# Kernel optimization log

Measured on AMD Instinct MI355X. Metric: run time of the kernel, lower is better.

Reference implementation:

```python
import jax, jax.numpy as jnp
import numpy as np

DAMPENING = 50.0
THR = 1.0
TAU = 10.0
DECAY = float(np.exp(-1.0 / TAU))
V_MIN = -1.0


@jax.custom_vjp
def spike_fn(v_scaled):
    # Heaviside spike with surrogate (triangular) gradient
    return (v_scaled > 0.0).astype(v_scaled.dtype)

def _spike_fwd(v_scaled):
    return spike_fn(v_scaled), v_scaled

def _spike_bwd(v_scaled, dy):
    return (dy * DAMPENING * jnp.maximum(0.0, 1.0 - jnp.abs(v_scaled)),)

spike_fn.defvjp(_spike_fwd, _spike_bwd)


def setup_inputs() -> dict:
    key = jax.random.key(0)
    T, B, N_IN, N = 256, 32, 256, 2048
    ks = jax.random.split(key, 4)
    x = jax.random.normal(ks[0], (T, B, N_IN), jnp.float32)
    W_in = jax.random.normal(ks[1], (N_IN, N), jnp.float32) * (1.0 / np.sqrt(N_IN))
    b = jnp.zeros((N,), jnp.float32)
    # original uses stddev 1/sqrt(n_in) for Bernoulli_weights as well
    W_bern = jax.random.normal(ks[2], (N, N), jnp.float32) * (1.0 / np.sqrt(N_IN))
    random_indices = jax.random.randint(ks[3], (T, N), 0, N)
    return {"x": x, "W_in": W_in, "b": b, "W_bern": W_bern,
            "random_indices": random_indices}


def reference(x, W_in, b, W_bern, random_indices):
    # x: [T, B, n_in]; states v, z2: [B, n]
    B, N = x.shape[1], W_in.shape[1]
    v0 = jnp.zeros((B, N), x.dtype)
    z2_0 = jnp.zeros((B, N), x.dtype)  # old_spike state (unused in math, as in original)

    def step(carry, inp):
        v, _old_z2 = carry
        xt, idx = inp
        i_in = xt @ W_in + b                               # [B, n]
        new_v = jnp.clip(DECAY * v + i_in, V_MIN, THR + 0.01)
        z = spike_fn(new_v - THR)                          # spikes [B, n]
        new_v = jnp.where(z > 0.0, V_MIN, new_v)           # hard reset
        z2 = jnp.take(z @ W_bern, idx, axis=1)             # stochastic projection + column gather
        return (new_v, z2), (z, new_v, z2)

    _, (zs, vs, z2s) = jax.lax.scan(step, (v0, z2_0), (x, random_indices))
    return jnp.stack([zs, vs, z2s], axis=0)  # [3, T, B, n]
```

## Files before the change

kernel.cpp:

```cpp
#include <hip/hip_runtime.h>
#include <hip/hip_bf16.h>
#include <stdint.h>


#define T_STEPS 256
#define BATCH   32
#define NIN     256
#define NN      2048
#define BN_FLAT (BATCH * NN)
#define TBN     (T_STEPS * BATCH * NN)
#define MROWS   (T_STEPS * BATCH)

typedef __attribute__((ext_vector_type(4))) float fx4;
typedef __attribute__((ext_vector_type(4))) int   ix4;

__device__ __forceinline__ void gll16(const void* g, void* l) {
  typedef __attribute__((address_space(1))) void gvoid_t;
  typedef __attribute__((address_space(3))) void lvoid_t;
  __builtin_amdgcn_global_load_lds((gvoid_t*)(g), (lvoid_t*)(l), 16, 0, 0);
}

__device__ __forceinline__ void mfma16(fx4& d, ix4 a, ix4 b) {
  asm volatile("v_mfma_f32_16x16x32_bf16 %0, %1, %2, %0" : "+v"(d) : "v"(a), "v"(b));
}

__global__ __launch_bounds__(256) void xt_k(const float* __restrict__ X,
                                            float* __restrict__ Xt) {
  __shared__ float tile[32][33];
  const int m0 = blockIdx.x << 5, k0 = blockIdx.y << 5;
  const int tx = threadIdx.x, ty = threadIdx.y;
#pragma unroll
  for (int i = 0; i < 32; i += 8)
    tile[ty + i][tx] = X[(size_t)(m0 + ty + i) * NIN + k0 + tx];
  __syncthreads();
#pragma unroll
  for (int i = 0; i < 32; i += 8)
    Xt[(size_t)(k0 + ty + i) * MROWS + m0 + tx] = tile[tx][ty + i];
}

__global__ __launch_bounds__(256) void wt_convert(const float* __restrict__ W,
                                                  __hip_bfloat16* __restrict__ Wt) {
  __shared__ float tile[32][33];
  const int k0 = blockIdx.y << 5, n0 = blockIdx.x << 5;
  const int tx = threadIdx.x, ty = threadIdx.y;
#pragma unroll
  for (int i = 0; i < 32; i += 8)
    tile[ty + i][tx] = W[(size_t)(k0 + ty + i) * NN + n0 + tx];
  __syncthreads();
#pragma unroll
  for (int i = 0; i < 32; i += 8)
    Wt[(size_t)(n0 + ty + i) * NN + k0 + tx] = __float2bfloat16(tile[tx][ty + i]);
}

__global__ __launch_bounds__(256) void in_gemm(const float* __restrict__ Xt,
                                               const float* __restrict__ Wi,
                                               const float* __restrict__ bias,
                                               float* __restrict__ I) {
  __shared__ __align__(16) float As[16 * 64];
  __shared__ __align__(16) float Bs[16 * 128];
  const int tid = threadIdx.x;
  const int tm = tid >> 4;
  const int tn = tid & 15;
  const int m0 = blockIdx.x * 64, n0 = blockIdx.y * 128;

  fx4 acc[4][2] = {};

  const float* gA = Xt + (size_t)(tid >> 4) * MROWS + m0 + (tid & 15) * 4;
  const float* gB = Wi + (size_t)(tid >> 5) * NN + n0 + (tid & 31) * 4;
  char* lA = (char*)As + tid * 16;
  char* lB = (char*)Bs + tid * 16;

  for (int k0 = 0; k0 < NIN; k0 += 16) {
    gll16(gA, lA);
    gll16(gB, lB);
    gll16(gB + 8 * NN, lB + 4096);
    gA += (size_t)16 * MROWS;
    gB += (size_t)16 * NN;
    __syncthreads();
#pragma unroll
    for (int kk = 0; kk < 16; ++kk) {
      fx4 a  = *(const fx4*)&As[kk * 64 + tm * 4];
      fx4 b0 = *(const fx4*)&Bs[kk * 128 + tn * 4];
      fx4 b1 = *(const fx4*)&Bs[kk * 128 + 64 + tn * 4];
#pragma unroll
      for (int r = 0; r < 4; ++r)
#pragma unroll
        for (int c = 0; c < 4; ++c) {
          acc[r][0][c] = fmaf(a[r], b0[c], acc[r][0][c]);
          acc[r][1][c] = fmaf(a[r], b1[c], acc[r][1][c]);
        }
    }
    __syncthreads();
  }

#pragma unroll
  for (int r = 0; r < 4; ++r) {
    const size_t row = (size_t)(m0 + tm * 4 + r) * NN;
    fx4 r0, r1;
#pragma unroll
    for (int c = 0; c < 4; ++c) {
      r0[c] = acc[r][0][c] + bias[n0 + tn * 4 + c];
      r1[c] = acc[r][1][c] + bias[n0 + 64 + tn * 4 + c];
    }
    *(fx4*)&I[row + n0 + tn * 4] = r0;
    *(fx4*)&I[row + n0 + 64 + tn * 4] = r1;
  }
}

__device__ __forceinline__ void scan_body(float* zs, float* vsout,
                                          const float* I, __hip_bfloat16* Zb) {
  const int nid = blockIdx.x * 256 + threadIdx.x;
  float v = 0.f;
  for (int t0 = 0; t0 < T_STEPS; t0 += 8) {
    float iin[8];
#pragma unroll
    for (int u = 0; u < 8; ++u)
      iin[u] = I[(size_t)(t0 + u) * BN_FLAT + nid];
#pragma unroll
    for (int u = 0; u < 8; ++u) {
      float nv = __fadd_rn(__fmul_rn(0.9048374180359595f, v), iin[u]);
      nv = fminf(fmaxf(nv, -1.0f), 1.01f);
      const bool sp = nv > 1.0f;
      const float z = sp ? 1.0f : 0.0f;
      nv = sp ? -1.0f : nv;
      const size_t off = (size_t)(t0 + u) * BN_FLAT + nid;
      zs[off] = z;
      vsout[off] = nv;
      Zb[off] = __float2bfloat16(z);
      v = nv;
    }
  }
}

__global__ __launch_bounds__(256) void scan_sep(float* __restrict__ out,
                                                const float* __restrict__ I,
                                                __hip_bfloat16* __restrict__ Zb) {
  scan_body(out, out + (size_t)TBN, I, Zb);
}

__global__ __launch_bounds__(256) void scan_inp(float* out, __hip_bfloat16* Zb) {
  scan_body(out, out + (size_t)TBN, out + (size_t)TBN, Zb);
}

__global__ __launch_bounds__(512, 2) void bern_gemm(const __hip_bfloat16* __restrict__ Z,
                                                    const __hip_bfloat16* __restrict__ Wt,
                                                    float* __restrict__ Y) {
  __shared__ __align__(16) char lds[131072];
  const int tid = threadIdx.x;
  const int l = tid & 63, wid = tid >> 6;
  const int wr = wid >> 2, wc = wid & 3;
  const int l15 = l & 15, l4 = l >> 4;
  const int swz = (l & 7) << 4;
  const int colp[2] = { (l4 * 16) ^ swz, (64 + l4 * 16) ^ swz };
  const int m0 = blockIdx.x * 256, n0 = blockIdx.y * 256;
  const int aoff = wr * 16384 + l15 * 128;
  const int boff = 65536 + (wc >> 1) * 16384 + ((wc & 1) * 64 + l15) * 128;
  const int colsel = ((tid & 7) ^ ((tid >> 3) & 7)) * 16;
  const char* gA_ = (const char*)Z + ((size_t)(m0 + (tid >> 3)) << 12) + colsel;
  const char* gB_ = (const char*)Wt + ((size_t)(n0 + (tid >> 3)) << 12) + colsel;

  fx4 acc[8][4] = {};
  ix4 af[4][2], bf[4][2];

#define STAGE_A(tt, h)                                                       \
  do {                                                                       \
    const char* g = gA_ + ((size_t)((h) * 128) << 12) + (size_t)(tt) * 128;  \
    char* d = lds + (((tt) & 1) * 32768) + (h) * 16384 + tid * 16;           \
    gll16(g, d);                                                             \
    gll16(g + ((size_t)64 << 12), d + 8192);                                 \
  } while (0)
#define STAGE_B(tt, h)                                                       \
  do {                                                                       \
    const char* g = gB_ + ((size_t)((h) * 128) << 12) + (size_t)(tt) * 128;  \
    char* d = lds + 65536 + (((tt) & 1) * 32768) + (h) * 16384 + tid * 16;   \
    gll16(g, d);                                                             \
    gll16(g + ((size_t)64 << 12), d + 8192);                                 \
  } while (0)
#define LDA(mh)                                                              \
  _Pragma("unroll") for (int mf = 0; mf < 4; ++mf)                           \
    _Pragma("unroll") for (int ks = 0; ks < 2; ++ks)                         \
      af[mf][ks] = *(const ix4*)(lb + aoff + ((mh)*4 + mf) * 2048 + colp[ks]);
#define LDB(nh)                                                              \
  _Pragma("unroll") for (int nf = 0; nf < 2; ++nf)                           \
    _Pragma("unroll") for (int ks = 0; ks < 2; ++ks)                         \
      bf[(nh)*2 + nf][ks] = *(const ix4*)(lb + boff + ((nh)*2 + nf) * 2048 + colp[ks]);
#define MFMA_QUAD(mh, nh)                                                    \
  do {                                                                       \
    __builtin_amdgcn_s_setprio(1);                                           \
    _Pragma("unroll") for (int ks = 0; ks < 2; ++ks)                         \
      _Pragma("unroll") for (int mf = 0; mf < 4; ++mf)                       \
        _Pragma("unroll") for (int nf = 0; nf < 2; ++nf)                     \
          mfma16(acc[(mh)*4 + mf][(nh)*2 + nf], af[mf][ks], bf[(nh)*2 + nf][ks]); \
    __builtin_amdgcn_s_setprio(0);                                           \
  } while (0)
#define SBAR asm volatile("s_barrier" ::: "memory")

  STAGE_A(0, 0); STAGE_A(0, 1); STAGE_B(0, 0); STAGE_B(0, 1);
  STAGE_B(1, 0); STAGE_B(1, 1);
  asm volatile("s_waitcnt vmcnt(4)" ::: "memory");
  SBAR;

  for (int t = 0; t < 32; ++t) {
    const char* lb = lds + (t & 1) * 32768;
    LDA(0); LDB(0);
    if (t < 31) STAGE_A(t + 1, 0);
    SBAR;
    asm volatile("s_waitcnt lgkmcnt(0)" ::: "memory");
    MFMA_QUAD(0, 0);
    SBAR;
    LDB(1);
    if (t < 31) STAGE_A(t + 1, 1);
    SBAR;
    asm volatile("s_waitcnt lgkmcnt(0)" ::: "memory");
    MFMA_QUAD(0, 1);
    SBAR;
    LDA(1);
    if (t < 30) STAGE_B(t + 2, 0);
    SBAR;
    asm volatile("s_waitcnt lgkmcnt(0)" ::: "memory");
    MFMA_QUAD(1, 0);
    SBAR;
    if (t < 30) STAGE_B(t + 2, 1);
    SBAR;
    MFMA_QUAD(1, 1);
    if (t < 30) asm volatile("s_waitcnt vmcnt(4)" ::: "memory");
    else        asm volatile("s_waitcnt vmcnt(0)" ::: "memory");
    SBAR;
  }

#undef STAGE_A
#undef STAGE_B
#undef LDA
#undef LDB
#undef MFMA_QUAD
#undef SBAR

  const int crow = l4 * 4;
#pragma unroll
  for (int MF = 0; MF < 8; ++MF)
#pragma unroll
    for (int NF = 0; NF < 4; ++NF)
#pragma unroll
      for (int j = 0; j < 4; ++j) {
        const int r = m0 + wr * 128 + MF * 16 + crow + j;
        const int c = n0 + wc * 64 + NF * 16 + l15;
        Y[(size_t)r * NN + c] = acc[MF][NF][j];
      }
}

__global__ __launch_bounds__(256) void gather_k(float* __restrict__ Y,
                                                const int* __restrict__ ridx) {
  __shared__ __align__(16) float rowbuf[NN];
  const int tb = blockIdx.x;
  const int t = tb >> 5;
  float* yrow = Y + (size_t)tb * NN;
  const int tid = threadIdx.x;
#pragma unroll
  for (int i = 0; i < 2; ++i) {
    int u = tid + i * 256;
    ((fx4*)rowbuf)[u] = ((const fx4*)yrow)[u];
  }
  __syncthreads();
  const int* ir = ridx + t * NN;
#pragma unroll
  for (int i = 0; i < 8; ++i) {
    int j = tid + i * 256;
    yrow[j] = rowbuf[ir[j]];
  }
}

extern "C" void kernel_launch(void* const* d_in, const int* in_sizes, int n_in,
                              void* d_out, int out_size, void* d_ws, size_t ws_size,
                              hipStream_t stream) {
  const float* x      = (const float*)d_in[0];
  const float* W_in   = (const float*)d_in[1];
  const float* bias   = (const float*)d_in[2];
  const float* W_bern = (const float*)d_in[3];
  const int*   ridx   = (const int*)d_in[4];
  float* out = (float*)d_out;
  char* ws = (char*)d_ws;

  __hip_bfloat16* Wt = (__hip_bfloat16*)ws;
  __hip_bfloat16* Zb = (__hip_bfloat16*)(ws + (size_t)8388608);
  const size_t offI = 41943040;
  const bool sep = ws_size >= (size_t)109051904;
  float* Ibuf = sep ? (float*)(ws + offI) : (out + (size_t)TBN);

  float* Xt = out;

  xt_k<<<dim3(256, 8), dim3(32, 8), 0, stream>>>(x, Xt);
  wt_convert<<<dim3(64, 64), dim3(32, 8), 0, stream>>>(W_bern, Wt);
  in_gemm<<<dim3(128, 16), dim3(256), 0, stream>>>(Xt, W_in, bias, Ibuf);
  if (sep)
    scan_sep<<<dim3(256), dim3(256), 0, stream>>>(out, Ibuf, Zb);
  else
    scan_inp<<<dim3(256), dim3(256), 0, stream>>>(out, Zb);
  bern_gemm<<<dim3(32, 8), dim3(512), 0, stream>>>(Zb, Wt, out + (size_t)2 * TBN);
  gather_k<<<dim3(8192), dim3(256), 0, stream>>>(out + (size_t)2 * TBN, ridx);
}
```

Baseline: 238.4 us.

## Drop X transpose kernel and read X rows directly in input GEMM

Removes the separate transpose kernel for X and restructures the FP32 input GEMM so each wave owns 8 rows of X, loaded as wave-uniform vector reads straight from global memory. Each lane computes 4 output columns over 8 rows, with a 256-wide W_in tile staged in LDS. This saves one kernel launch and a full read and write of X. The cost is that A operands now come from scalar/global loads rather than LDS, and the tile shape changes from 64x128 to 32x256.

```diff
diff --git a/kernel.cpp b/kernel.cpp
--- a/kernel.cpp
+++ b/kernel.cpp
@@ -24,20 +24,6 @@
   asm volatile("v_mfma_f32_16x16x32_bf16 %0, %1, %2, %0" : "+v"(d) : "v"(a), "v"(b));
 }
 
-__global__ __launch_bounds__(256) void xt_k(const float* __restrict__ X,
-                                            float* __restrict__ Xt) {
-  __shared__ float tile[32][33];
-  const int m0 = blockIdx.x << 5, k0 = blockIdx.y << 5;
-  const int tx = threadIdx.x, ty = threadIdx.y;
-#pragma unroll
-  for (int i = 0; i < 32; i += 8)
-    tile[ty + i][tx] = X[(size_t)(m0 + ty + i) * NIN + k0 + tx];
-  __syncthreads();
-#pragma unroll
-  for (int i = 0; i < 32; i += 8)
-    Xt[(size_t)(k0 + ty + i) * MROWS + m0 + tx] = tile[tx][ty + i];
-}
-
 __global__ __launch_bounds__(256) void wt_convert(const float* __restrict__ W,
                                                   __hip_bfloat16* __restrict__ Wt) {
   __shared__ float tile[32][33];
@@ -52,58 +38,54 @@
     Wt[(size_t)(n0 + ty + i) * NN + k0 + tx] = __float2bfloat16(tile[tx][ty + i]);
 }
 
-__global__ __launch_bounds__(256) void in_gemm(const float* __restrict__ Xt,
+__global__ __launch_bounds__(256) void in_gemm(const float* __restrict__ X,
                                                const float* __restrict__ Wi,
                                                const float* __restrict__ bias,
                                                float* __restrict__ I) {
-  __shared__ __align__(16) float As[16 * 64];
-  __shared__ __align__(16) float Bs[16 * 128];
+  __shared__ __align__(16) float Bs[16 * 256];
   const int tid = threadIdx.x;
-  const int tm = tid >> 4;
-  const int tn = tid & 15;
-  const int m0 = blockIdx.x * 64, n0 = blockIdx.y * 128;
-
-  fx4 acc[4][2] = {};
-
-  const float* gA = Xt + (size_t)(tid >> 4) * MROWS + m0 + (tid & 15) * 4;
-  const float* gB = Wi + (size_t)(tid >> 5) * NN + n0 + (tid & 31) * 4;
-  char* lA = (char*)As + tid * 16;
+  const int lane = tid & 63;
+  const int w = tid >> 6;
+  const int m0 = blockIdx.x * 32, n0 = blockIdx.y * 256;
+  const int wrow = __builtin_amdgcn_readfirstlane(m0 + 8 * w);
+  const float* aP = X + (size_t)wrow * NIN;
+
+  fx4 acc[8] = {};
+
+  const float* gB = Wi + (size_t)(tid >> 6) * NN + n0 + (tid & 63) * 4;
   char* lB = (char*)Bs + tid * 16;
 
   for (int k0 = 0; k0 < NIN; k0 += 16) {
-    gll16(gA, lA);
-    gll16(gB, lB);
-    gll16(gB + 8 * NN, lB + 4096);
-    gA += (size_t)16 * MROWS;
+#pragma unroll
+    for (int j = 0; j < 4; ++j)
+      gll16(gB + (size_t)(4 * j) * NN, lB + 4096 * j);
     gB += (size_t)16 * NN;
     __syncthreads();
 #pragma unroll
-    for (int kk = 0; kk < 16; ++kk) {
-      fx4 a  = *(const fx4*)&As[kk * 64 + tm * 4];
-      fx4 b0 = *(const fx4*)&Bs[kk * 128 + tn * 4];
-      fx4 b1 = *(const fx4*)&Bs[kk * 128 + 64 + tn * 4];
-#pragma unroll
-      for (int r = 0; r < 4; ++r)
-#pragma unroll
-        for (int c = 0; c < 4; ++c) {
-          acc[r][0][c] = fmaf(a[r], b0[c], acc[r][0][c]);
-          acc[r][1][c] = fmaf(a[r], b1[c], acc[r][1][c]);
-        }
+    for (int kq = 0; kq < 4; ++kq) {
+      fx4 ar[8];
+#pragma unroll
+      for (int r = 0; r < 8; ++r)
+        ar[r] = *(const fx4*)&aP[r * NIN + k0 + kq * 4];
+#pragma unroll
+      for (int kk = 0; kk < 4; ++kk) {
+        fx4 b = *(const fx4*)&Bs[(kq * 4 + kk) * 256 + lane * 4];
+#pragma unroll
+        for (int r = 0; r < 8; ++r)
+#pragma unroll
+          for (int c = 0; c < 4; ++c)
+            acc[r][c] = fmaf(ar[r][kk], b[c], acc[r][c]);
+      }
     }
     __syncthreads();
   }
 
 #pragma unroll
-  for (int r = 0; r < 4; ++r) {
-    const size_t row = (size_t)(m0 + tm * 4 + r) * NN;
-    fx4 r0, r1;
-#pragma unroll
-    for (int c = 0; c < 4; ++c) {
-      r0[c] = acc[r][0][c] + bias[n0 + tn * 4 + c];
-      r1[c] = acc[r][1][c] + bias[n0 + 64 + tn * 4 + c];
-    }
-    *(fx4*)&I[row + n0 + tn * 4] = r0;
-    *(fx4*)&I[row + n0 + 64 + tn * 4] = r1;
+  for (int r = 0; r < 8; ++r) {
+    fx4 res;
+#pragma unroll
+    for (int c = 0; c < 4; ++c) res[c] = acc[r][c] + bias[n0 + lane * 4 + c];
+    *(fx4*)&I[(size_t)(wrow + r) * NN + n0 + lane * 4] = res;
   }
 }
 
@@ -286,11 +268,8 @@
   const bool sep = ws_size >= (size_t)109051904;
   float* Ibuf = sep ? (float*)(ws + offI) : (out + (size_t)TBN);
 
-  float* Xt = out;
-
-  xt_k<<<dim3(256, 8), dim3(32, 8), 0, stream>>>(x, Xt);
   wt_convert<<<dim3(64, 64), dim3(32, 8), 0, stream>>>(W_bern, Wt);
-  in_gemm<<<dim3(128, 16), dim3(256), 0, stream>>>(Xt, W_in, bias, Ibuf);
+  in_gemm<<<dim3(256, 8), dim3(256), 0, stream>>>(x, W_in, bias, Ibuf);
   if (sep)
     scan_sep<<<dim3(256), dim3(256), 0, stream>>>(out, Ibuf, Zb);
   else
```

After: 230.4 us. 3.4% less time.
